# Kernel tuning notes

Measured on AMD Instinct MI355X. Metric: run time of the kernel, lower is better.

## Reference

```python
import jax, jax.numpy as jnp
import numpy as np

B, T, V, E, U, OUT = 1024, 64, 30, 128, 512, 20


def _lstm(x, W, Uh, b, reverse=False, return_seq=True):
    """Keras-style LSTM (gate order i,f,g,o). x: [B,T,D]. Returns [B,T,U] or [B,U]."""
    nu = Uh.shape[0]
    if reverse:
        x = x[:, ::-1]
    xz = jnp.einsum('btd,dg->btg', x, W) + b  # [B,T,4U] input projection, precomputed

    def step(carry, z_t):
        h, c = carry
        z = z_t + h @ Uh
        i, f, g, o = jnp.split(z, 4, axis=-1)
        c = jax.nn.sigmoid(f) * c + jax.nn.sigmoid(i) * jnp.tanh(g)
        h = jax.nn.sigmoid(o) * jnp.tanh(c)
        return (h, c), h

    bsz = x.shape[0]
    init = (jnp.zeros((bsz, nu), x.dtype), jnp.zeros((bsz, nu), x.dtype))
    (h_last, _), hs = jax.lax.scan(step, init, jnp.swapaxes(xz, 0, 1))
    if return_seq:
        hs = jnp.swapaxes(hs, 0, 1)  # [B,T,U]
        if reverse:
            hs = hs[:, ::-1]
        return hs
    return h_last


def setup_inputs() -> dict:
    key = jax.random.key(0)
    ks = jax.random.split(key, 14)
    f32 = jnp.float32

    def n(k, shape, s=0.05):
        return jax.random.normal(k, shape, f32) * s

    G = 4 * U
    return {
        'x': jax.random.randint(ks[0], (B, T), 0, V, dtype=jnp.int32),
        'emb': n(ks[1], (V, E)),
        # layer 1 forward / backward directions
        'W1f': n(ks[2], (E, G)), 'U1f': n(ks[3], (U, G)), 'b1f': jnp.zeros((G,), f32),
        'W1b': n(ks[4], (E, G)), 'U1b': n(ks[5], (U, G)), 'b1b': jnp.zeros((G,), f32),
        # layer 2 forward / backward directions (input dim = 2U from concat)
        'W2f': n(ks[6], (2 * U, G)), 'U2f': n(ks[7], (U, G)), 'b2f': jnp.zeros((G,), f32),
        'W2b': n(ks[8], (2 * U, G)), 'U2b': n(ks[9], (U, G)), 'b2b': jnp.zeros((G,), f32),
        # dense head
        'Wd': n(ks[10], (2 * U, 2 * U)), 'bd': jnp.zeros((2 * U,), f32),
        'Wo': n(ks[11], (2 * U, OUT)), 'bo': jnp.zeros((OUT,), f32),
    }


def reference(x, emb, W1f, U1f, b1f, W1b, U1b, b1b,
              W2f, U2f, b2f, W2b, U2b, b2b, Wd, bd, Wo, bo):
    e = emb[x]  # [B,T,E] embedding lookup
    # Bidirectional LSTM 1, return_sequences=True, concat merge -> [B,T,2U]
    h1 = jnp.concatenate([
        _lstm(e, W1f, U1f, b1f),
        _lstm(e, W1b, U1b, b1b, reverse=True),
    ], axis=-1)
    # Bidirectional LSTM 2, return_sequences=False -> [B,2U]
    h2 = jnp.concatenate([
        _lstm(h1, W2f, U2f, b2f, return_seq=False),
        _lstm(h1, W2b, U2b, b2b, reverse=True, return_seq=False),
    ], axis=-1)
    d = jax.nn.relu(h2 @ Wd + bd)  # Dense(2U, relu)
    return d @ Wo + bo             # Dense(output_len), [B,OUT]
```

## Files before the change

kernel.cpp:

```cpp
#include <hip/hip_runtime.h>
#include <hip/hip_bf16.h>

typedef __hip_bfloat16 bf16;
typedef __attribute__((ext_vector_type(4))) float f32x4;
typedef __attribute__((ext_vector_type(8))) short s16x8;

__device__ __forceinline__ float sigf(float x) {
    return 1.0f / (1.0f + __expf(-x));
}
__device__ __forceinline__ float tanh_f(float x) {
    float ax = fabsf(x);
    float e = __expf(-2.0f * ax);
    float r = (1.0f - e) / (1.0f + e);
    return x < 0.0f ? -r : r;
}

#define GLL16(src, ldst)                                                      \
    __builtin_amdgcn_global_load_lds(                                         \
        (const __attribute__((address_space(1))) void*)(src),                 \
        (__attribute__((address_space(3))) void*)(ldst), 16, 0, 0)

#define PIPE_BAR(N)                                                           \
    do {                                                                      \
        asm volatile("s_waitcnt vmcnt(" #N ") lgkmcnt(0)" ::: "memory");      \
        __builtin_amdgcn_s_barrier();                                         \
        __builtin_amdgcn_sched_barrier(0);                                    \
    } while (0)

__global__ void k_embw(const float* __restrict__ emb,
                       const float* __restrict__ W1f, const float* __restrict__ b1f,
                       const float* __restrict__ W1b, const float* __restrict__ b1b,
                       float* __restrict__ embW) {
    int c = blockIdx.x * 256 + threadIdx.x;
    int v = blockIdx.y;
    int d = blockIdx.z;
    const float* W = d ? W1b : W1f;
    const float* b = d ? b1b : b1f;
    float acc = b[c];
    const float* er = emb + v * 128;
#pragma unroll 8
    for (int e = 0; e < 128; ++e) acc += er[e] * W[e * 2048 + c];
    int n = ((c & 511) << 2) | (c >> 9);
    embW[(d * 30 + v) * 2048 + n] = acc;
}

__global__ void k_b2r(const float* __restrict__ b2f, const float* __restrict__ b2b,
                      float* __restrict__ dst) {
    int i = blockIdx.x * 256 + threadIdx.x;
    int d = i >> 11, n = i & 2047;
    int c = ((n & 3) << 9) | (n >> 2);
    dst[i] = (d ? b2b : b2f)[c];
}

template<int REORDER, int XOR>
__global__ void k_trans(const float* __restrict__ src, bf16* __restrict__ dst,
                        int ncols, int kpitch, int koff) {
    __shared__ float tile[64][65];
    int k0 = blockIdx.x * 64;
    int c0 = blockIdx.y * 64;
    int tid = threadIdx.x;
#pragma unroll
    for (int i = 0; i < 16; ++i) {
        int seg = tid + i * 256;
        int r = seg >> 6, cc = seg & 63;
        tile[r][cc] = src[(size_t)(k0 + r) * ncols + c0 + cc];
    }
    __syncthreads();
#pragma unroll
    for (int i = 0; i < 16; ++i) {
        int seg = tid + i * 256;
        int nl = seg >> 6, kl = seg & 63;
        int c = c0 + nl;
        int n = REORDER ? (((c & 511) << 2) | (c >> 9)) : c;
        int kabs = koff + k0 + kl;
        int ks = XOR ? (kabs ^ ((n & 7) << 3)) : kabs;
        dst[(size_t)n * kpitch + ks] = __float2bfloat16(tile[kl][nl]);
    }
}

template<int MODE>
__global__ __launch_bounds__(256, 2)
void k_step(const bf16* __restrict__ A1, const bf16* __restrict__ A2,
            const bf16* __restrict__ Bt, const float* __restrict__ table,
            const int* __restrict__ xin, float* __restrict__ c_st,
            bf16* __restrict__ h_out, bf16* __restrict__ h1s, int t)
{
    constexpr int NCH = (MODE == 0) ? 8 : 24;
    constexpr int BP  = (MODE == 0) ? 512 : 1536;

    extern __shared__ __align__(16) short ldss[];

    const int tid  = threadIdx.x;
    const int lane = tid & 63;
    const int wv   = tid >> 6;
    const int wm   = wv << 5;

    const int xcd = blockIdx.x & 7, idx = blockIdx.x >> 3;
    const int n0  = ((xcd << 2) | (idx >> 4)) << 6;
    const int m0  = (idx & 15) << 7;

    const int dir = (m0 >= 1024);
    const int t_a = dir ? 63 - t : t;
    const int rl  = lane & 15;
    const int q8  = (lane >> 4) << 3;
    const int q4  = (lane >> 4) << 2;
    const int xk  = (rl & 7) << 3;
    const int u0  = n0 >> 2;

    const char* a1b;
    if constexpr (MODE == 1)
        a1b = (const char*)(A1 + ((size_t)t_a << 20) + ((size_t)(m0 & 1023) << 10));
    else
        a1b = (const char*)(A1 + (size_t)m0 * 512);
    const char* const btb = (const char*)(Bt + ((size_t)dir * 2048 + n0) * BP);
    const char* const a2b = (const char*)A2;

    auto stage = [&](int c, int buf) {
        char* base = (char*)ldss + buf * 24576;
#pragma unroll
        for (int i = 0; i < 4; ++i) {
            const int u = i * 256 + tid;
            const int r = u >> 3, j = u & 7;
            const char* src;
            if constexpr (MODE == 0)
                src = a1b + r * 1024 + c * 128 + j * 16;
            else
                src = (c < 16) ? a1b + r * 2048 + c * 128 + j * 16
                               : a2b + (size_t)(m0 + r) * 1024 + (c - 16) * 128 + j * 16;
            GLL16(src, base + (i * 256 + wv * 64) * 16);
        }
#pragma unroll
        for (int i = 0; i < 2; ++i) {
            const int u = i * 256 + tid;
            const int r = u >> 3, j = u & 7;
            GLL16(btb + (size_t)r * (BP * 2) + c * 128 + j * 16,
                  base + 16384 + (i * 256 + wv * 64) * 16);
        }
    };

    f32x4 acc[2][4];
#pragma unroll
    for (int i = 0; i < 2; ++i)
#pragma unroll
        for (int j = 0; j < 4; ++j) acc[i][j] = (f32x4){0.f, 0.f, 0.f, 0.f};

    auto compute = [&](const short* as) {
        const short* bs = as + 8192;
        __builtin_amdgcn_s_setprio(1);
#pragma unroll
        for (int ks = 0; ks < 2; ++ks) {
            const int eo = ((ks << 5) + q8) ^ xk;
            s16x8 af[2], bq[4];
#pragma unroll
            for (int f = 0; f < 2; ++f)
                af[f] = *(const s16x8*)&as[(wm + f * 16 + rl) * 64 + eo];
#pragma unroll
            for (int f = 0; f < 4; ++f)
                bq[f] = *(const s16x8*)&bs[(f * 16 + rl) * 64 + eo];
#pragma unroll
            for (int fm = 0; fm < 2; ++fm)
#pragma unroll
                for (int fn = 0; fn < 4; ++fn)
                    acc[fm][fn] = __builtin_amdgcn_mfma_f32_16x16x32_bf16(
                        af[fm], bq[fn], acc[fm][fn], 0, 0, 0);
        }
        __builtin_amdgcn_s_setprio(0);
    };

    stage(0, 0);
    stage(1, 1);

    int cb = 0, sb = 2;
#pragma unroll 1
    for (int c = 0; c < NCH - 1; ++c) {
        PIPE_BAR(6);
        if (c + 2 < NCH) stage(c + 2, sb);
        compute(ldss + cb * 12288);
        cb = (cb == 2) ? 0 : cb + 1;
        sb = (sb == 2) ? 0 : sb + 1;
    }
    PIPE_BAR(0);
    compute(ldss + cb * 12288);

    float* z = (float*)ldss;
    __syncthreads();
#pragma unroll
    for (int fm = 0; fm < 2; ++fm)
#pragma unroll
        for (int fn = 0; fn < 4; ++fn) {
            const int zr = wm + fm * 16 + q4;
            const int zc = fn * 16 + rl;
#pragma unroll
            for (int r = 0; r < 4; ++r)
                z[(zr + r) * 68 + zc] = acc[fm][fn][r];
        }
    __syncthreads();
#pragma unroll 2
    for (int j = 0; j < 8; ++j) {
        const int cid = j * 256 + tid;
        const int ml = cid >> 4;
        const int ul = cid & 15;
        const int mg = m0 + ml;
        const int b  = mg & 1023;
        float4 z4 = *(float4*)&z[ml * 68 + (ul << 2)];
        const float* tab;
        if constexpr (MODE == 0) {
            const int v = xin[(b << 6) + t_a];
            tab = table + (size_t)(dir * 30 + v) * 2048;
        } else {
            tab = table + dir * 2048;
        }
        const float4 tv = *(const float4*)&tab[n0 + (ul << 2)];
        const float zi = z4.x + tv.x, zf = z4.y + tv.y;
        const float zg = z4.z + tv.z, zo = z4.w + tv.w;
        const float ig = sigf(zi), fg = sigf(zf);
        const float gg = tanh_f(zg), og = sigf(zo);
        const int u = u0 + ul;
        const size_t cu = (size_t)mg * 512 + u;
        const float cn = fg * c_st[cu] + ig * gg;
        c_st[cu] = cn;
        const float h = og * tanh_f(cn);
        const int us = u ^ ((mg & 7) << 3);
        h_out[(size_t)mg * 512 + us] = __float2bfloat16(h);
        if constexpr (MODE == 0) {
            const int col = (((dir << 9) | u) ^ ((b & 7) << 3));
            h1s[(((size_t)t_a << 10) + b) * 1024 + col] = __float2bfloat16(h);
        }
    }
}

__global__ __launch_bounds__(256, 2)
void k_dense(const bf16* __restrict__ hin, const bf16* __restrict__ Bt,
             const float* __restrict__ bd, bf16* __restrict__ dbuf)
{
    __shared__ __align__(16) short ldss[32768];
    const int tid  = threadIdx.x;
    const int lane = tid & 63;
    const int wv   = tid >> 6;
    const int wm   = (wv >> 1) << 6;
    const int wn   = (wv & 1) << 6;
    const int n0   = (blockIdx.x & 7) << 7;
    const int m0   = (blockIdx.x >> 3) << 7;

    const char* const a1b = (const char*)(hin + (size_t)m0 * 512);
    const char* const a2b = (const char*)(hin + (size_t)1024 * 512);
    const char* const btb = (const char*)(Bt + (size_t)n0 * 1024);

    auto stage = [&](int c, int buf) {
#pragma unroll
        for (int i = 0; i < 4; ++i) {
            const int u = i * 256 + tid;
            const int r = u >> 3, j = u & 7;
            const char* src = (c < 8)
                ? a1b + r * 1024 + c * 128 + j * 16
                : a2b + (size_t)(m0 + r) * 1024 + (c - 8) * 128 + j * 16;
            GLL16(src, (char*)ldss + buf * 16384 + (i * 256 + wv * 64) * 16);
        }
#pragma unroll
        for (int i = 0; i < 4; ++i) {
            const int u = i * 256 + tid;
            const int r = u >> 3, j = u & 7;
            GLL16(btb + (size_t)r * 2048 + c * 128 + j * 16,
                  (char*)ldss + 32768 + buf * 16384 + (i * 256 + wv * 64) * 16);
        }
    };

    f32x4 acc[4][4];
#pragma unroll
    for (int i = 0; i < 4; ++i)
#pragma unroll
        for (int j = 0; j < 4; ++j) acc[i][j] = (f32x4){0.f, 0.f, 0.f, 0.f};

    stage(0, 0);
    const int rl = lane & 15;
    const int q8 = (lane >> 4) << 3;
    const int xk = (rl & 7) << 3;

#pragma unroll 2
    for (int c = 0; c < 16; ++c) {
        __syncthreads();
        if (c + 1 < 16) stage(c + 1, (c + 1) & 1);
        const short* as = ldss + (c & 1) * 8192;
        const short* bs = ldss + 16384 + (c & 1) * 8192;
#pragma unroll
        for (int ks = 0; ks < 2; ++ks) {
            const int eo = ((ks << 5) + q8) ^ xk;
            s16x8 af[4], bq[4];
#pragma unroll
            for (int f = 0; f < 4; ++f)
                af[f] = *(const s16x8*)&as[(wm + f * 16 + rl) * 64 + eo];
#pragma unroll
            for (int f = 0; f < 4; ++f)
                bq[f] = *(const s16x8*)&bs[(wn + f * 16 + rl) * 64 + eo];
#pragma unroll
            for (int fm = 0; fm < 4; ++fm)
#pragma unroll
                for (int fn = 0; fn < 4; ++fn)
                    acc[fm][fn] = __builtin_amdgcn_mfma_f32_16x16x32_bf16(
                        af[fm], bq[fn], acc[fm][fn], 0, 0, 0);
        }
    }

#pragma unroll
    for (int fn = 0; fn < 4; ++fn) {
        const int col = n0 + wn + fn * 16 + rl;
        const float bdv = bd[col];
#pragma unroll
        for (int fm = 0; fm < 4; ++fm) {
            const int rb = m0 + wm + fm * 16 + ((lane >> 4) << 2);
#pragma unroll
            for (int r = 0; r < 4; ++r) {
                float v = acc[fm][fn][r] + bdv;
                dbuf[(size_t)(rb + r) * 1024 + col] =
                    __float2bfloat16(v > 0.f ? v : 0.f);
            }
        }
    }
}

__global__ __launch_bounds__(256)
void k_out(const bf16* __restrict__ dbuf, const float* __restrict__ Wo,
           const float* __restrict__ bo, float* __restrict__ out) {
    int b = blockIdx.x, tid = threadIdx.x;
    int wv = tid >> 6, lane = tid & 63;
    float acc[5] = {0.f, 0.f, 0.f, 0.f, 0.f};
    for (int kk = 0; kk < 1024; kk += 64) {
        float a = __bfloat162float(dbuf[b * 1024 + kk + lane]);
#pragma unroll
        for (int j = 0; j < 5; ++j)
            acc[j] += a * Wo[(kk + lane) * 20 + wv + j * 4];
    }
#pragma unroll
    for (int j = 0; j < 5; ++j) {
        float s = acc[j];
        for (int off = 32; off; off >>= 1) s += __shfl_down(s, off, 64);
        if (lane == 0) out[b * 20 + wv + j * 4] = s + bo[wv + j * 4];
    }
}

extern "C" void kernel_launch(void* const* d_in, const int* in_sizes, int n_in,
                              void* d_out, int out_size, void* d_ws, size_t ws_size,
                              hipStream_t stream) {
    const int*   x   = (const int*)  d_in[0];
    const float* emb = (const float*)d_in[1];
    const float* W1f = (const float*)d_in[2];
    const float* U1f = (const float*)d_in[3];
    const float* b1f = (const float*)d_in[4];
    const float* W1b = (const float*)d_in[5];
    const float* U1b = (const float*)d_in[6];
    const float* b1b = (const float*)d_in[7];
    const float* W2f = (const float*)d_in[8];
    const float* U2f = (const float*)d_in[9];
    const float* b2f = (const float*)d_in[10];
    const float* W2b = (const float*)d_in[11];
    const float* U2b = (const float*)d_in[12];
    const float* b2b = (const float*)d_in[13];
    const float* Wd  = (const float*)d_in[14];
    const float* bd  = (const float*)d_in[15];
    const float* Wo  = (const float*)d_in[16];
    const float* bo  = (const float*)d_in[17];

    char* ws = (char*)d_ws;
    float* embW = (float*)(ws + 0);
    float* b2r  = (float*)(ws + 491520);
    bf16* Ut1   = (bf16*)(ws + 507904);
    bf16* BigBt = (bf16*)(ws + 4702208);
    bf16* Wdt   = (bf16*)(ws + 17285120);
    bf16* hA    = (bf16*)(ws + 19382272);
    bf16* hB    = (bf16*)(ws + 21479424);
    float* cst  = (float*)(ws + 23576576);
    bf16* dbuf  = (bf16*)(ws + 27770880);
    bf16* h1seq = (bf16*)(ws + 29868032);

    hipFuncSetAttribute((const void*)k_step<0>,
                        hipFuncAttributeMaxDynamicSharedMemorySize, 73728);
    hipFuncSetAttribute((const void*)k_step<1>,
                        hipFuncAttributeMaxDynamicSharedMemorySize, 73728);

    k_embw<<<dim3(8, 30, 2), 256, 0, stream>>>(emb, W1f, b1f, W1b, b1b, embW);
    k_b2r<<<16, 256, 0, stream>>>(b2f, b2b, b2r);
    k_trans<1, 1><<<dim3(8, 32), 256, 0, stream>>>(U1f, Ut1,              2048, 512, 0);
    k_trans<1, 1><<<dim3(8, 32), 256, 0, stream>>>(U1b, Ut1 + 2048 * 512, 2048, 512, 0);
    k_trans<1, 1><<<dim3(16, 32), 256, 0, stream>>>(W2f, BigBt,                2048, 1536, 0);
    k_trans<1, 1><<<dim3(8, 32), 256, 0, stream>>>(U2f, BigBt,                2048, 1536, 1024);
    k_trans<1, 1><<<dim3(16, 32), 256, 0, stream>>>(W2b, BigBt + 2048 * 1536, 2048, 1536, 0);
    k_trans<1, 1><<<dim3(8, 32), 256, 0, stream>>>(U2b, BigBt + 2048 * 1536, 2048, 1536, 1024);
    k_trans<0, 1><<<dim3(16, 16), 256, 0, stream>>>(Wd, Wdt, 1024, 1024, 0);

    hipMemsetAsync(hA, 0, (size_t)2048 * 512 * sizeof(bf16), stream);
    hipMemsetAsync(cst, 0, (size_t)2048 * 512 * sizeof(float), stream);
    bf16 *hin = hA, *hout = hB;
    for (int t = 0; t < 64; ++t) {
        k_step<0><<<512, 256, 73728, stream>>>(
            hin, (const bf16*)nullptr, Ut1, embW, x, cst, hout, h1seq, t);
        bf16* tmp = hin; hin = hout; hout = tmp;
    }

    hipMemsetAsync(hin, 0, (size_t)2048 * 512 * sizeof(bf16), stream);
    hipMemsetAsync(cst, 0, (size_t)2048 * 512 * sizeof(float), stream);
    for (int t = 0; t < 64; ++t) {
        k_step<1><<<512, 256, 73728, stream>>>(
            h1seq, hin, BigBt, b2r, (const int*)nullptr, cst, hout,
            (bf16*)nullptr, t);
        bf16* tmp = hin; hin = hout; hout = tmp;
    }

    k_dense<<<64, 256, 0, stream>>>(hin, Wdt, bd, dbuf);
    k_out<<<1024, 256, 0, stream>>>(dbuf, Wo, bo, (float*)d_out);
}
```

Baseline: 2.204 ms.

## Widen layer-2 step tile to 128 columns and vectorize the gate epilogue

For the layer-2 recurrent step, each block now computes a 128x128 output tile with a 2x2 wave layout instead of 128x64. This halves the grid to 256 blocks and raises shared memory per block to 96KB, so the shared A operand is reused across more columns. The gate epilogue for both modes now processes four hidden units per thread, using vector loads and stores for c state, h, and the sequence buffer. The trade-off is fewer blocks (occupancy 1) and a larger z scratch, which may leave CUs underused on a 256-CU-class device.

```diff
diff --git a/kernel.cpp b/kernel.cpp
--- a/kernel.cpp
+++ b/kernel.cpp
@@ -4,6 +4,7 @@
 typedef __hip_bfloat16 bf16;
 typedef __attribute__((ext_vector_type(4))) float f32x4;
 typedef __attribute__((ext_vector_type(8))) short s16x8;
+typedef __attribute__((ext_vector_type(4))) short s16x4;
 
 __device__ __forceinline__ float sigf(float x) {
     return 1.0f / (1.0f + __expf(-x));
@@ -79,7 +80,7 @@
 }
 
 template<int MODE>
-__global__ __launch_bounds__(256, 2)
+__global__ __launch_bounds__(256, MODE == 0 ? 2 : 1)
 void k_step(const bf16* __restrict__ A1, const bf16* __restrict__ A2,
             const bf16* __restrict__ Bt, const float* __restrict__ table,
             const int* __restrict__ xin, float* __restrict__ c_st,
@@ -87,17 +88,26 @@
 {
     constexpr int NCH = (MODE == 0) ? 8 : 24;
     constexpr int BP  = (MODE == 0) ? 512 : 1536;
+    constexpr int NT  = (MODE == 0) ? 64 : 128;
+    constexpr int CHS = (MODE == 0) ? 12288 : 16384;
 
     extern __shared__ __align__(16) short ldss[];
 
     const int tid  = threadIdx.x;
     const int lane = tid & 63;
     const int wv   = tid >> 6;
-    const int wm   = wv << 5;
-
-    const int xcd = blockIdx.x & 7, idx = blockIdx.x >> 3;
-    const int n0  = ((xcd << 2) | (idx >> 4)) << 6;
-    const int m0  = (idx & 15) << 7;
+
+    int n0, m0;
+    {
+        const int xcd = blockIdx.x & 7, idx = blockIdx.x >> 3;
+        if constexpr (MODE == 0) {
+            n0 = ((xcd << 2) | (idx >> 4)) << 6;
+            m0 = (idx & 15) << 7;
+        } else {
+            n0 = ((xcd << 1) | (idx >> 4)) << 7;
+            m0 = (idx & 15) << 7;
+        }
+    }
 
     const int dir = (m0 >= 1024);
     const int t_a = dir ? 63 - t : t;
@@ -116,7 +126,7 @@
     const char* const a2b = (const char*)A2;
 
     auto stage = [&](int c, int buf) {
-        char* base = (char*)ldss + buf * 24576;
+        char* base = (char*)ldss + buf * (CHS * 2);
 #pragma unroll
         for (int i = 0; i < 4; ++i) {
             const int u = i * 256 + tid;
@@ -130,7 +140,7 @@
             GLL16(src, base + (i * 256 + wv * 64) * 16);
         }
 #pragma unroll
-        for (int i = 0; i < 2; ++i) {
+        for (int i = 0; i < NT / 32; ++i) {
             const int u = i * 256 + tid;
             const int r = u >> 3, j = u & 7;
             GLL16(btb + (size_t)r * (BP * 2) + c * 128 + j * 16,
@@ -138,9 +148,13 @@
         }
     };
 
-    f32x4 acc[2][4];
-#pragma unroll
-    for (int i = 0; i < 2; ++i)
+    constexpr int FM = (MODE == 0) ? 2 : 4;
+    const int wm = (MODE == 0) ? (wv << 5) : ((wv >> 1) << 6);
+    const int wn = (MODE == 0) ? 0 : ((wv & 1) << 6);
+
+    f32x4 acc[FM][4];
+#pragma unroll
+    for (int i = 0; i < FM; ++i)
 #pragma unroll
         for (int j = 0; j < 4; ++j) acc[i][j] = (f32x4){0.f, 0.f, 0.f, 0.f};
 
@@ -150,15 +164,15 @@
 #pragma unroll
         for (int ks = 0; ks < 2; ++ks) {
             const int eo = ((ks << 5) + q8) ^ xk;
-            s16x8 af[2], bq[4];
-#pragma unroll
-            for (int f = 0; f < 2; ++f)
+            s16x8 af[FM], bq[4];
+#pragma unroll
+            for (int f = 0; f < FM; ++f)
                 af[f] = *(const s16x8*)&as[(wm + f * 16 + rl) * 64 + eo];
 #pragma unroll
             for (int f = 0; f < 4; ++f)
-                bq[f] = *(const s16x8*)&bs[(f * 16 + rl) * 64 + eo];
-#pragma unroll
-            for (int fm = 0; fm < 2; ++fm)
+                bq[f] = *(const s16x8*)&bs[(wn + f * 16 + rl) * 64 + eo];
+#pragma unroll
+            for (int fm = 0; fm < FM; ++fm)
 #pragma unroll
                 for (int fn = 0; fn < 4; ++fn)
                     acc[fm][fn] = __builtin_amdgcn_mfma_f32_16x16x32_bf16(
@@ -173,58 +187,73 @@
     int cb = 0, sb = 2;
 #pragma unroll 1
     for (int c = 0; c < NCH - 1; ++c) {
-        PIPE_BAR(6);
+        if constexpr (MODE == 0) PIPE_BAR(6); else PIPE_BAR(8);
         if (c + 2 < NCH) stage(c + 2, sb);
-        compute(ldss + cb * 12288);
+        compute(ldss + cb * CHS);
         cb = (cb == 2) ? 0 : cb + 1;
         sb = (sb == 2) ? 0 : sb + 1;
     }
     PIPE_BAR(0);
-    compute(ldss + cb * 12288);
-
+    compute(ldss + cb * CHS);
+
+    constexpr int ZP    = NT + 4;
+    constexpr int TPR   = NT / 16;
+    constexpr int EITER = 128 * TPR / 256;
     float* z = (float*)ldss;
     __syncthreads();
 #pragma unroll
-    for (int fm = 0; fm < 2; ++fm)
+    for (int fm = 0; fm < FM; ++fm)
 #pragma unroll
         for (int fn = 0; fn < 4; ++fn) {
             const int zr = wm + fm * 16 + q4;
-            const int zc = fn * 16 + rl;
+            const int zc = wn + fn * 16 + rl;
 #pragma unroll
             for (int r = 0; r < 4; ++r)
-                z[(zr + r) * 68 + zc] = acc[fm][fn][r];
+                z[(zr + r) * ZP + zc] = acc[fm][fn][r];
         }
     __syncthreads();
-#pragma unroll 2
-    for (int j = 0; j < 8; ++j) {
+#pragma unroll
+    for (int j = 0; j < EITER; ++j) {
         const int cid = j * 256 + tid;
-        const int ml = cid >> 4;
-        const int ul = cid & 15;
+        const int ml = cid / TPR;
+        const int ug = (cid & (TPR - 1)) << 2;
         const int mg = m0 + ml;
         const int b  = mg & 1023;
-        float4 z4 = *(float4*)&z[ml * 68 + (ul << 2)];
+        const float* zrow = &z[ml * ZP + (ug << 2)];
         const float* tab;
         if constexpr (MODE == 0) {
             const int v = xin[(b << 6) + t_a];
-            tab = table + (size_t)(dir * 30 + v) * 2048;
+            tab = table + (size_t)(dir * 30 + v) * 2048 + n0 + (ug << 2);
         } else {
-            tab = table + dir * 2048;
-        }
-        const float4 tv = *(const float4*)&tab[n0 + (ul << 2)];
-        const float zi = z4.x + tv.x, zf = z4.y + tv.y;
-        const float zg = z4.z + tv.z, zo = z4.w + tv.w;
-        const float ig = sigf(zi), fg = sigf(zf);
-        const float gg = tanh_f(zg), og = sigf(zo);
-        const int u = u0 + ul;
-        const size_t cu = (size_t)mg * 512 + u;
-        const float cn = fg * c_st[cu] + ig * gg;
-        c_st[cu] = cn;
-        const float h = og * tanh_f(cn);
-        const int us = u ^ ((mg & 7) << 3);
-        h_out[(size_t)mg * 512 + us] = __float2bfloat16(h);
+            tab = table + dir * 2048 + n0 + (ug << 2);
+        }
+        const size_t cbase = (size_t)mg * 512 + u0 + ug;
+        f32x4 c4 = *(f32x4*)&c_st[cbase];
+        f32x4 cn4;
+        float hv[4];
+#pragma unroll
+        for (int k = 0; k < 4; ++k) {
+            const f32x4 zq = *(const f32x4*)&zrow[k * 4];
+            const float4 tq = *(const float4*)&tab[k * 4];
+            const float ig = sigf(zq[0] + tq.x);
+            const float fg = sigf(zq[1] + tq.y);
+            const float gg = tanh_f(zq[2] + tq.z);
+            const float og = sigf(zq[3] + tq.w);
+            cn4[k] = fg * c4[k] + ig * gg;
+            hv[k] = og * tanh_f(cn4[k]);
+        }
+        *(f32x4*)&c_st[cbase] = cn4;
+        s16x4 hq;
+#pragma unroll
+        for (int k = 0; k < 4; ++k) {
+            bf16 hb = __float2bfloat16(hv[k]);
+            hq[k] = *(short*)&hb;
+        }
+        const int us = (u0 + ug) ^ ((mg & 7) << 3);
+        *(s16x4*)&h_out[(size_t)mg * 512 + us] = hq;
         if constexpr (MODE == 0) {
-            const int col = (((dir << 9) | u) ^ ((b & 7) << 3));
-            h1s[(((size_t)t_a << 10) + b) * 1024 + col] = __float2bfloat16(h);
+            const int col = (((dir << 9) | (u0 + ug)) ^ ((b & 7) << 3));
+            *(s16x4*)&h1s[(((size_t)t_a << 10) + b) * 1024 + col] = hq;
         }
     }
 }
@@ -375,7 +404,7 @@
     hipFuncSetAttribute((const void*)k_step<0>,
                         hipFuncAttributeMaxDynamicSharedMemorySize, 73728);
     hipFuncSetAttribute((const void*)k_step<1>,
-                        hipFuncAttributeMaxDynamicSharedMemorySize, 73728);
+                        hipFuncAttributeMaxDynamicSharedMemorySize, 98304);
 
     k_embw<<<dim3(8, 30, 2), 256, 0, stream>>>(emb, W1f, b1f, W1b, b1b, embW);
     k_b2r<<<16, 256, 0, stream>>>(b2f, b2b, b2r);
@@ -399,7 +428,7 @@
     hipMemsetAsync(hin, 0, (size_t)2048 * 512 * sizeof(bf16), stream);
     hipMemsetAsync(cst, 0, (size_t)2048 * 512 * sizeof(float), stream);
     for (int t = 0; t < 64; ++t) {
-        k_step<1><<<512, 256, 73728, stream>>>(
+        k_step<1><<<256, 256, 98304, stream>>>(
             h1seq, hin, BigBt, b2r, (const int*)nullptr, cst, hout,
             (bf16*)nullptr, t);
         bf16* tmp = hin; hin = hout; hout = tmp;
```

Measured after the change: 2.233 ms. No clear change (+1.3%).
